# Performance work log

Hardware: AMD Instinct MI355X
Metric: run time of the kernel (lower is better)

The kernel has to match this reference:

```python
import jax, jax.numpy as jnp
import numpy as np

KER = 8  # patch size used by unfold/fold
EPS = 1e-5


def _gelu(x):
    return jax.nn.gelu(x, approximate=False)  # torch nn.GELU default (exact erf)


def _conv(x, w, b):
    # x: [B,C,H,W], w: [O,I,kh,kw]
    y = jax.lax.conv_general_dilated(x, w, (1, 1), 'SAME',
                                     dimension_numbers=('NCHW', 'OIHW', 'NCHW'))
    return y + b[None, :, None, None]


def _unfold_t(x):
    # F.unfold(k=8, s=8).transpose(1,2): [B,C,H,W] -> [B, L, C*k*k]
    B, C, H, W = x.shape
    Hp, Wp = H // KER, W // KER
    x = x.reshape(B, C, Hp, KER, Wp, KER)
    x = x.transpose(0, 2, 4, 1, 3, 5)  # [B,Hp,Wp,C,k,k]
    return x.reshape(B, Hp * Wp, C * KER * KER)


def _fold(y, H, W):
    # inverse of unfold (non-overlapping): [B,L,C*k*k] -> [B,C,H,W]
    B, L, D = y.shape
    Hp, Wp = H // KER, W // KER
    C = D // (KER * KER)
    y = y.reshape(B, Hp, Wp, C, KER, KER).transpose(0, 3, 1, 4, 2, 5)
    return y.reshape(B, C, H, W)


def _bn1d(x, gamma, beta):
    # BatchNorm1d (training-mode batch stats) on [B, C, L]: stats over (B, L)
    m = x.mean(axis=(0, 2), keepdims=True)
    v = x.var(axis=(0, 2), keepdims=True)  # biased variance, matches torch fwd
    return (x - m) * jax.lax.rsqrt(v + EPS) * gamma[None, :, None] + beta[None, :, None]


def setup_inputs() -> dict:
    key = jax.random.key(0)
    ks = jax.random.split(key, 12)
    B, C, H, W = 4, 64, 256, 256
    dq = KER * KER * C  # 4096

    def n(k, shape, scale=0.02):
        return jax.random.normal(k, shape, jnp.float32) * scale

    return {
        'feat': jax.random.normal(ks[0], (B, C, H, W), jnp.float32),
        'w_enc': n(ks[1], (C, C, 3, 3)), 'b_enc': jnp.zeros((C,), jnp.float32),
        'w_kc': n(ks[2], (C, C, 3, 3)), 'b_kc': jnp.zeros((C,), jnp.float32),
        'w_vc': n(ks[3], (C, C, 3, 3)), 'b_vc': jnp.zeros((C,), jnp.float32),
        'wq': n(ks[4], (1024, dq)), 'bq': jnp.zeros((1024,), jnp.float32),
        'wk': n(ks[5], (1024, dq)), 'bk': jnp.zeros((1024,), jnp.float32),
        'gq': jnp.ones((1024,), jnp.float32), 'betaq': jnp.zeros((1024,), jnp.float32),
        'gk': jnp.ones((1024,), jnp.float32), 'betak': jnp.zeros((1024,), jnp.float32),
        'w_f1': n(ks[6], (4 * C, C, 1, 1)), 'b_f1': jnp.zeros((4 * C,), jnp.float32),
        'w_f2': n(ks[7], (C, 4 * C, 1, 1)), 'b_f2': jnp.zeros((C,), jnp.float32),
    }


def reference(feat, w_enc, b_enc, w_kc, b_kc, w_vc, b_vc, wq, bq, wk, bk,
              gq, betaq, gk, betak, w_f1, b_f1, w_f2, b_f2):
    H, W = feat.shape[-2:]
    refer = _gelu(_conv(feat, w_enc, b_enc))
    feat_k = _gelu(_conv(feat, w_kc, b_kc))
    feat_v = _gelu(_conv(feat, w_vc, b_vc))

    q_un = _unfold_t(refer)   # [B,L,4096]
    k_un = _unfold_t(feat_k)
    v_un = _unfold_t(feat_v)

    # Linear -> BN1d over 1024 channels (transpose dance as in the torch code)
    qp = _bn1d((q_un @ wq.T + bq).transpose(0, 2, 1), gq, betaq).transpose(0, 2, 1)  # [B,L,1024]
    kp = _bn1d((k_un @ wk.T + bk).transpose(0, 2, 1), gk, betak).transpose(0, 2, 1)  # [B,L,1024]

    scale = jnp.sqrt(jnp.asarray(qp.shape[2], qp.dtype))
    scores = jnp.einsum('bld,bmd->blm', qp, kp) / scale  # [B,L,L]
    attn = jax.nn.softmax(scores, axis=2)
    out = jnp.einsum('blm,bmd->bld', attn, v_un)  # [B,L,4096]

    out = _fold(out, H, W)  # [B,C,H,W]
    ff = _gelu(_conv(out, w_f1, b_f1))
    ff = _gelu(_conv(ff, w_f2, b_f2))
    return ff + feat
```

## Files before the change

### kernel.cpp

```cpp
#include <hip/hip_runtime.h>
#include <hip/hip_bf16.h>

typedef unsigned short u16;
typedef __attribute__((ext_vector_type(8))) short short8v;
typedef __attribute__((ext_vector_type(8))) unsigned short u16x8;
typedef __attribute__((ext_vector_type(4))) float f32x4;

#define HWPIX 65536

__device__ __forceinline__ float bfbits2f(u16 u) {
  return __uint_as_float(((unsigned)u) << 16);
}
__device__ __forceinline__ float4 ld4bf(const u16* p) {
  ushort4 u = *(const ushort4*)(const void*)p;
  return make_float4(bfbits2f(u.x), bfbits2f(u.y), bfbits2f(u.z), bfbits2f(u.w));
}
__device__ __forceinline__ u16 f2bf(float f) {
  union { __hip_bfloat16 h; u16 u; } c;
  c.h = __float2bfloat16(f);
  return c.u;
}
__device__ __forceinline__ float gelu_f(float x) {
  float z = 0.79788456f * x * (1.0f + 0.044715f * x * x);
  float e = __expf(2.0f * z);
  float th = 1.0f - 2.0f * __builtin_amdgcn_rcpf(e + 1.0f);
  return 0.5f * x * (1.0f + th);
}
__device__ __forceinline__ u16x8 bn8(u16x8 v, const float* __restrict__ sc,
                                     const float* __restrict__ sh, int kk) {
  float4 s0 = *(const float4*)&sc[kk], s1 = *(const float4*)&sc[kk + 4];
  float4 t0 = *(const float4*)&sh[kk], t1 = *(const float4*)&sh[kk + 4];
  u16x8 r;
  r[0] = f2bf(bfbits2f(v[0]) * s0.x + t0.x); r[1] = f2bf(bfbits2f(v[1]) * s0.y + t0.y);
  r[2] = f2bf(bfbits2f(v[2]) * s0.z + t0.z); r[3] = f2bf(bfbits2f(v[3]) * s0.w + t0.w);
  r[4] = f2bf(bfbits2f(v[4]) * s1.x + t1.x); r[5] = f2bf(bfbits2f(v[5]) * s1.y + t1.y);
  r[6] = f2bf(bfbits2f(v[6]) * s1.z + t1.z); r[7] = f2bf(bfbits2f(v[7]) * s1.w + t1.w);
  return r;
}

__launch_bounds__(256)
__global__ void nhwc_k(const float* __restrict__ x, u16* __restrict__ y) {
  __shared__ float tile[64][65];
  const int t = threadIdx.x;
  const int xs = blockIdx.x << 6, yy = blockIdx.y, b = blockIdx.z;
#pragma unroll
  for (int it = 0; it < 4; ++it) {
    const int idx = t + it * 256;
    const int c = idx >> 4, seg = (idx & 15) << 2;
    float4 v = *(const float4*)&x[(((size_t)(b * 64 + c)) << 16) + yy * 256 + xs + seg];
    tile[c][seg] = v.x; tile[c][seg + 1] = v.y; tile[c][seg + 2] = v.z; tile[c][seg + 3] = v.w;
  }
  __syncthreads();
#pragma unroll
  for (int it = 0; it < 4; ++it) {
    const int idx = t + it * 256;
    const int cs = (idx & 15) << 2, px = idx >> 4;
    ushort4 r;
    r.x = f2bf(tile[cs + 0][px]); r.y = f2bf(tile[cs + 1][px]);
    r.z = f2bf(tile[cs + 2][px]); r.w = f2bf(tile[cs + 3][px]);
    *(ushort4*)&y[(((size_t)((b * 256 + yy) * 256 + xs + px)) << 6) + cs] = r;
  }
}

__launch_bounds__(256)
__global__ void wcvt2_k(const float* __restrict__ s0, u16* __restrict__ d0,
                        const float* __restrict__ s1, u16* __restrict__ d1) {
  const float* src = blockIdx.y ? s1 : s0;
  u16* dst = blockIdx.y ? d1 : d0;
  const int i = (blockIdx.x * 256 + threadIdx.x) << 2;
  float4 v = *(const float4*)&src[i];
  ushort4 r;
  r.x = f2bf(v.x); r.y = f2bf(v.y); r.z = f2bf(v.z); r.w = f2bf(v.w);
  *(ushort4*)&dst[i] = r;
}

__launch_bounds__(256)
__global__ void wprep_k(const float* __restrict__ w0, const float* __restrict__ w1,
                        const float* __restrict__ w2, const float* __restrict__ b0,
                        const float* __restrict__ b1, const float* __restrict__ b2,
                        const float* __restrict__ wf1, const float* __restrict__ wf2,
                        u16* __restrict__ wT, float* __restrict__ bias192,
                        u16* __restrict__ wf1b, u16* __restrict__ wf2b) {
  const int t = threadIdx.x;
  const int bx = blockIdx.x;
  if (bx >= 497) {
    const int e = (bx - 497) * 256 + t;
    wf2b[e] = f2bf(wf2[e]);
    return;
  }
  if (bx >= 433) {
    const int e = (bx - 433) * 256 + t;
    wf1b[e] = f2bf(wf1[e]);
    return;
  }
  if (bx == 432) {
    if (t < 192) {
      const float* bp = (t < 64) ? b0 : (t < 128) ? b1 : b2;
      bias192[t] = bp[t & 63];
    }
    return;
  }
  const int e = bx * 256 + t;
  const int pos = e / 12288, rem = e % 12288;
  const int n = rem >> 6, ic = rem & 63;
  const int conv = n >> 6, oc = n & 63;
  const float* wp = (conv == 0) ? w0 : (conv == 1) ? w1 : w2;
  wT[e] = f2bf(wp[(oc * 64 + ic) * 9 + pos]);
}

__launch_bounds__(256)
__global__ void convmfma_k(const u16* __restrict__ featb, const u16* __restrict__ wT,
                           const float* __restrict__ bias192, u16* __restrict__ qun,
                           u16* __restrict__ kun, u16* __restrict__ vT) {
  __shared__ u16 As[128 * 40];
  __shared__ u16 Bs[192 * 40];
  const int tid = threadIdx.x;
  const int lin = blockIdx.x;
  const int virt = (lin & 7) * 256 + (lin >> 3);
  const int b = virt >> 9, yy = (virt >> 1) & 255, x0 = (virt & 1) << 7;
  const int lane = tid & 63, w = tid >> 6;
  const int wm = w >> 1, wn = w & 1;

  const int arow = tid >> 1, acs = (tid & 1) << 4;
  const int brow0 = tid >> 2, bseg0 = (tid & 3) << 3;

  f32x4 acc[4][6] = {};
  const int kc = (lane >> 4) << 3;
  const int afr = wm * 64 + (lane & 15);
  const int bfr0 = wn * 96 + (lane & 15);

  for (int s = 0; s < 18; ++s) {
    const int pos = s >> 1, half = (s & 1) << 5;
    const int dy = pos / 3, dx = pos % 3;
    {
      const int yp = yy + dy - 1;
      const int xp = x0 + arow + dx - 1;
      u16x8 pA0{}, pA1{};
      if ((unsigned)yp < 256u && (unsigned)xp < 256u) {
        const u16* src = featb + (((size_t)((b * 256 + yp) * 256 + xp)) << 6) + half + acs;
        pA0 = *(const u16x8*)src;
        pA1 = *(const u16x8*)(src + 8);
      }
      *(u16x8*)&As[arow * 40 + acs] = pA0;
      *(u16x8*)&As[arow * 40 + acs + 8] = pA1;
    }
    {
      const u16* wb = wT + (size_t)pos * 12288 + half;
      *(u16x8*)&Bs[(brow0 + 0) * 40 + bseg0] = *(const u16x8*)&wb[(brow0 + 0) * 64 + bseg0];
      *(u16x8*)&Bs[(brow0 + 64) * 40 + bseg0] = *(const u16x8*)&wb[(brow0 + 64) * 64 + bseg0];
      *(u16x8*)&Bs[(brow0 + 128) * 40 + bseg0] = *(const u16x8*)&wb[(brow0 + 128) * 64 + bseg0];
    }
    __syncthreads();
    short8v a[4], bf[6];
#pragma unroll
    for (int f = 0; f < 4; ++f) a[f] = *(const short8v*)&As[(afr + f * 16) * 40 + kc];
#pragma unroll
    for (int f = 0; f < 6; ++f) bf[f] = *(const short8v*)&Bs[(bfr0 + f * 16) * 40 + kc];
#pragma unroll
    for (int i = 0; i < 4; ++i)
#pragma unroll
      for (int j = 0; j < 6; ++j)
        acc[i][j] = __builtin_amdgcn_mfma_f32_16x16x32_bf16(a[i], bf[j], acc[i][j], 0, 0, 0);
    __syncthreads();
  }

  const int py = yy >> 3, ky = yy & 7;
  const int rp0 = wm * 64 + ((lane >> 4) << 2);
#pragma unroll
  for (int j = 0; j < 6; ++j) {
    const int colb = wn * 96 + j * 16;
    const int conv = colb >> 6;
    const int oc = (colb & 63) + (lane & 15);
    const float bj = bias192[colb + (lane & 15)];
#pragma unroll
    for (int i = 0; i < 4; ++i) {
      const int rp = rp0 + i * 16;
      const int xg = x0 + rp;
      const int px = xg >> 3, kx0 = xg & 7;
      float v0 = gelu_f(acc[i][j][0] + bj);
      float v1 = gelu_f(acc[i][j][1] + bj);
      float v2 = gelu_f(acc[i][j][2] + bj);
      float v3 = gelu_f(acc[i][j][3] + bj);
      const int d0 = (oc << 6) + (ky << 3) + kx0;
      if (conv < 2) {
        u16* dst = conv ? kun : qun;
        const size_t addr = (((size_t)((b << 10) + py * 32 + px)) << 12) + d0;
        ushort4 r4;
        r4.x = f2bf(v0); r4.y = f2bf(v1); r4.z = f2bf(v2); r4.w = f2bf(v3);
        *(ushort4*)&dst[addr] = r4;
      } else {
        const int m = py * 32 + px;
        const size_t base = (((size_t)(b * 4096 + d0)) << 10) + m;
        vT[base] = f2bf(v0);
        vT[base + 1024] = f2bf(v1);
        vT[base + 2048] = f2bf(v2);
        vT[base + 3072] = f2bf(v3);
      }
    }
  }
}

__launch_bounds__(256)
__global__ void bnpart_k(const u16* __restrict__ q, const u16* __restrict__ k,
                         float2* __restrict__ part) {
  const u16* x = blockIdx.y ? k : q;
  const int b = blockIdx.x, t = threadIdx.x;
  const int c = t << 2;
  float s0 = 0.f, s1 = 0.f, s2 = 0.f, s3 = 0.f;
  float q0 = 0.f, q1 = 0.f, q2 = 0.f, q3 = 0.f;
  const u16* base = x + ((size_t)b << 15) + c;
#pragma unroll 4
  for (int r = 0; r < 32; ++r) {
    float4 v = ld4bf(base + (r << 10));
    s0 += v.x; q0 += v.x * v.x;
    s1 += v.y; q1 += v.y * v.y;
    s2 += v.z; q2 += v.z * v.z;
    s3 += v.w; q3 += v.w * v.w;
  }
  float2* dst = part + (((size_t)(blockIdx.y * 128 + b)) << 10) + c;
  dst[0] = make_float2(s0, q0);
  dst[1] = make_float2(s1, q1);
  dst[2] = make_float2(s2, q2);
  dst[3] = make_float2(s3, q3);
}
__launch_bounds__(256)
__global__ void bnfin_k(const float2* __restrict__ part, const float* __restrict__ gq,
                        const float* __restrict__ betaq, const float* __restrict__ gk,
                        const float* __restrict__ betak, float* __restrict__ scq,
                        float* __restrict__ shq, float* __restrict__ sck,
                        float* __restrict__ shk) {
  const int n = blockIdx.x * 256 + threadIdx.x;
  const int y = blockIdx.y;
  const float2* p = part + (((size_t)(y * 128)) << 10) + n;
  float S = 0.f, S2 = 0.f;
  for (int i = 0; i < 128; ++i) {
    float2 v = p[(size_t)i << 10];
    S += v.x; S2 += v.y;
  }
  const float mean = S * (1.0f / 4096.0f);
  const float var = S2 * (1.0f / 4096.0f) - mean * mean;
  const float rstd = rsqrtf(var + 1e-5f);
  const float g = (y ? gk : gq)[n];
  const float be = (y ? betak : betaq)[n];
  const float sc = g * rstd;
  (y ? sck : scq)[n] = sc;
  (y ? shk : shq)[n] = be - mean * sc;
}

__launch_bounds__(256)
__global__ void softmax_k(u16* __restrict__ s) {
  u16* p = s + (size_t)blockIdx.x * 1024;
  const int tid = threadIdx.x;
  float4 v = ld4bf(p + (tid << 2));
  float mx = fmaxf(fmaxf(v.x, v.y), fmaxf(v.z, v.w));
#pragma unroll
  for (int off = 32; off > 0; off >>= 1) mx = fmaxf(mx, __shfl_xor(mx, off));
  __shared__ float red[8];
  if ((tid & 63) == 0) red[tid >> 6] = mx;
  __syncthreads();
  mx = fmaxf(fmaxf(red[0], red[1]), fmaxf(red[2], red[3]));
  float e0 = __expf(v.x - mx), e1 = __expf(v.y - mx), e2 = __expf(v.z - mx), e3 = __expf(v.w - mx);
  float sm = e0 + e1 + e2 + e3;
#pragma unroll
  for (int off = 32; off > 0; off >>= 1) sm += __shfl_xor(sm, off);
  if ((tid & 63) == 0) red[4 + (tid >> 6)] = sm;
  __syncthreads();
  sm = red[4] + red[5] + red[6] + red[7];
  float inv = 1.0f / sm;
  ushort4 r;
  r.x = f2bf(e0 * inv); r.y = f2bf(e1 * inv); r.z = f2bf(e2 * inv); r.w = f2bf(e3 * inv);
  *(ushort4*)&p[tid << 2] = r;
}

template <int MODE>
__launch_bounds__(512)
__global__ void mgemm8_k(const u16* __restrict__ Ap0, const u16* __restrict__ Bp0,
                         const float* __restrict__ sA, const float* __restrict__ hA,
                         const float* __restrict__ sB, const float* __restrict__ hB,
                         const float* __restrict__ bias0, u16* __restrict__ Cp0, int K,
                         const u16* __restrict__ Ap2, const u16* __restrict__ Bp2,
                         const float* __restrict__ bias2, u16* __restrict__ Cp2) {
  constexpr int SD = (MODE == 0) ? 4096 : 1024;
  __shared__ u16 As[2][128 * 72];
  __shared__ u16 Bs[2][128 * 72];
  const int tid = threadIdx.x;

  int bx, by, z;
  if constexpr (MODE == 2) {
    int lin = blockIdx.x + 32 * blockIdx.y + 256 * blockIdx.z;
    int sw = (lin & 7) * 128 + (lin >> 3);
    bx = sw & 31; by = (sw >> 5) & 7; z = sw >> 8;
  } else {
    bx = blockIdx.x; by = blockIdx.y; z = blockIdx.z;
  }
  const u16* Ap = Ap0;
  const u16* Bp = Bp0;
  const float* bias = bias0;
  u16* Cp = Cp0;
  if constexpr (MODE == 0) {
    if (z) { Ap = Ap2; Bp = Bp2; bias = bias2; Cp = Cp2; }
  }
  const int m0 = by * 128, n0 = bx * 128;
  const int lane = tid & 63, w = tid >> 6;
  const int wm = w >> 2, wn = w & 3;

  const int srow = tid >> 3;
  const int scol = (tid & 7) << 3;
  const size_t zoffA = (MODE == 0) ? 0 : ((size_t)z << 10);
  const size_t zoffB = (MODE == 0) ? 0 : (MODE == 1) ? ((size_t)z << 10) : ((size_t)z << 12);
  const u16* A0 = Ap + (zoffA + m0 + srow) * (size_t)SD + scol;
  const u16* A1 = A0 + (size_t)64 * SD;
  const u16* B0 = Bp + (zoffB + n0 + srow) * (size_t)SD + scol;
  const u16* B1 = B0 + (size_t)64 * SD;
  const int l0 = srow * 72 + scol;
  const int l1 = (srow + 64) * 72 + scol;

  const int NT = K >> 6;
  u16x8 pA0 = *(const u16x8*)A0;
  u16x8 pA1 = *(const u16x8*)A1;
  u16x8 pB0 = *(const u16x8*)B0;
  u16x8 pB1 = *(const u16x8*)B1;
  if constexpr (MODE == 1) {
    pA0 = bn8(pA0, sA, hA, scol); pA1 = bn8(pA1, sA, hA, scol);
    pB0 = bn8(pB0, sB, hB, scol); pB1 = bn8(pB1, sB, hB, scol);
  }
  *(u16x8*)&As[0][l0] = pA0; *(u16x8*)&As[0][l1] = pA1;
  *(u16x8*)&Bs[0][l0] = pB0; *(u16x8*)&Bs[0][l1] = pB1;
  __syncthreads();

  f32x4 acc[4][2] = {};
  int cur = 0;
  for (int t = 0; t < NT; ++t) {
    const int kn = (t + 1) << 6;
    if (t + 1 < NT) {
      pA0 = *(const u16x8*)(A0 + kn);
      pA1 = *(const u16x8*)(A1 + kn);
      pB0 = *(const u16x8*)(B0 + kn);
      pB1 = *(const u16x8*)(B1 + kn);
    }
    const u16* Asb = As[cur];
    const u16* Bsb = Bs[cur];
#pragma unroll
    for (int ks = 0; ks < 2; ++ks) {
      const int kc = ks * 32 + ((lane >> 4) << 3);
      short8v a[4], bfr[2];
#pragma unroll
      for (int f = 0; f < 4; ++f)
        a[f] = *(const short8v*)&Asb[(wm * 64 + (lane & 15) + f * 16) * 72 + kc];
#pragma unroll
      for (int f = 0; f < 2; ++f)
        bfr[f] = *(const short8v*)&Bsb[(wn * 32 + (lane & 15) + f * 16) * 72 + kc];
#pragma unroll
      for (int i = 0; i < 4; ++i)
#pragma unroll
        for (int j = 0; j < 2; ++j)
          acc[i][j] = __builtin_amdgcn_mfma_f32_16x16x32_bf16(a[i], bfr[j], acc[i][j], 0, 0, 0);
    }
    if (t + 1 < NT) {
      if constexpr (MODE == 1) {
        pA0 = bn8(pA0, sA, hA, kn + scol); pA1 = bn8(pA1, sA, hA, kn + scol);
        pB0 = bn8(pB0, sB, hB, kn + scol); pB1 = bn8(pB1, sB, hB, kn + scol);
      }
      *(u16x8*)&As[cur ^ 1][l0] = pA0; *(u16x8*)&As[cur ^ 1][l1] = pA1;
      *(u16x8*)&Bs[cur ^ 1][l0] = pB0; *(u16x8*)&Bs[cur ^ 1][l1] = pB1;
    }
    __syncthreads();
    cur ^= 1;
  }

  const int rowbase = m0 + wm * 64 + ((lane >> 4) << 2);
  const int colbase = n0 + wn * 32 + (lane & 15);
  if constexpr (MODE == 2) {
    const size_t coff = (size_t)(8 + 8 * z) * 524288;
    u16* C = Cp + coff;
#pragma unroll
    for (int j = 0; j < 2; ++j) {
      const int d = colbase + j * 16;
      const int c = d >> 6, ky = (d >> 3) & 7, kx = d & 7;
#pragma unroll
      for (int i = 0; i < 4; ++i)
#pragma unroll
        for (int r = 0; r < 4; ++r) {
          const int l = rowbase + i * 16 + r;
          const int p = (((l >> 5) << 3) + ky) * 256 + ((l & 31) << 3) + kx;
          C[((size_t)p << 6) + c] = f2bf(acc[i][j][r]);
        }
    }
  } else {
#pragma unroll
    for (int j = 0; j < 2; ++j) {
      const int col = colbase + j * 16;
      float bj = 0.f;
      if constexpr (MODE == 0) bj = bias[col];
#pragma unroll
      for (int i = 0; i < 4; ++i)
#pragma unroll
        for (int r = 0; r < 4; ++r) {
          const size_t row = (MODE == 1 ? ((size_t)z << 10) : 0) + rowbase + i * 16 + r;
          float v = (MODE == 0) ? (acc[i][j][r] + bj) : (acc[i][j][r] * 0.03125f);
          Cp[row * 1024 + col] = f2bf(v);
        }
    }
  }
}

__launch_bounds__(512)
__global__ void ffn_k(const u16* __restrict__ fold, const u16* __restrict__ w1b,
                      const u16* __restrict__ w2b, const float* __restrict__ b1,
                      const float* __restrict__ b2, const float* __restrict__ feat,
                      float* __restrict__ out) {
  extern __shared__ u16 sh[];
  u16* Ash = sh;
  u16* W1s = sh + 9216;
  u16* mids = sh;
  const int t = threadIdx.x;
  const int px0 = blockIdx.x << 7;
  const int z = blockIdx.y;
  const u16* fz = fold + ((size_t)z << 22);

  {
    const int row = t >> 2, cs = (t & 3) << 4;
    const u16* src = fz + (((size_t)(px0 + row)) << 6) + cs;
    *(u16x8*)&Ash[row * 72 + cs] = *(const u16x8*)src;
    *(u16x8*)&Ash[row * 72 + cs + 8] = *(const u16x8*)(src + 8);
  }
  {
    const int row = t >> 1, cs = (t & 1) << 5;
    const u16* src = w1b + (((size_t)row) << 6) + cs;
    *(u16x8*)&W1s[row * 72 + cs] = *(const u16x8*)src;
    *(u16x8*)&W1s[row * 72 + cs + 8] = *(const u16x8*)(src + 8);
    *(u16x8*)&W1s[row * 72 + cs + 16] = *(const u16x8*)(src + 16);
    *(u16x8*)&W1s[row * 72 + cs + 24] = *(const u16x8*)(src + 24);
  }
  __syncthreads();

  const int lane = t & 63, w = t >> 6;
  const int kc = (lane >> 4) << 3;
  const int mrow = w * 16 + (lane & 15);
  f32x4 acc1[16] = {};
  short8v a0 = *(const short8v*)&Ash[mrow * 72 + kc];
  short8v a1 = *(const short8v*)&Ash[mrow * 72 + 32 + kc];
#pragma unroll
  for (int n = 0; n < 16; ++n) {
    const int br = n * 16 + (lane & 15);
    short8v b0 = *(const short8v*)&W1s[br * 72 + kc];
    short8v bv = *(const short8v*)&W1s[br * 72 + 32 + kc];
    acc1[n] = __builtin_amdgcn_mfma_f32_16x16x32_bf16(a0, b0, acc1[n], 0, 0, 0);
    acc1[n] = __builtin_amdgcn_mfma_f32_16x16x32_bf16(a1, bv, acc1[n], 0, 0, 0);
  }
  __syncthreads();

  const int mrow0 = w * 16 + ((lane >> 4) << 2);
#pragma unroll
  for (int n = 0; n < 16; ++n) {
    const int col = n * 16 + (lane & 15);
    const float bj = b1[col];
#pragma unroll
    for (int r = 0; r < 4; ++r)
      mids[(mrow0 + r) * 264 + col] = f2bf(gelu_f(acc1[n][r] + bj));
  }
  __syncthreads();

  f32x4 acc2[4] = {};
#pragma unroll
  for (int ks = 0; ks < 8; ++ks) {
    short8v a2 = *(const short8v*)&mids[(w * 16 + (lane & 15)) * 264 + ks * 32 + kc];
#pragma unroll
    for (int n = 0; n < 4; ++n) {
      short8v bv = *(const short8v*)(const void*)&w2b[(size_t)(n * 16 + (lane & 15)) * 256 + ks * 32 + kc];
      acc2[n] = __builtin_amdgcn_mfma_f32_16x16x32_bf16(a2, bv, acc2[n], 0, 0, 0);
    }
  }
#pragma unroll
  for (int n = 0; n < 4; ++n) {
    const int oc = n * 16 + (lane & 15);
    const float bn = b2[oc];
    const int px = px0 + mrow0;
    const size_t base = (((size_t)(z * 64 + oc)) << 16) + px;
    float4 f = *(const float4*)&feat[base];
    float4 rv;
    rv.x = gelu_f(acc2[n][0] + bn) + f.x;
    rv.y = gelu_f(acc2[n][1] + bn) + f.y;
    rv.z = gelu_f(acc2[n][2] + bn) + f.z;
    rv.w = gelu_f(acc2[n][3] + bn) + f.w;
    *(float4*)&out[base] = rv;
  }
}

extern "C" void kernel_launch(void* const* d_in, const int* in_sizes, int n_in,
                              void* d_out, int out_size, void* d_ws, size_t ws_size,
                              hipStream_t stream) {
  const float* feat  = (const float*)d_in[0];
  const float* w_enc = (const float*)d_in[1];
  const float* b_enc = (const float*)d_in[2];
  const float* w_kc  = (const float*)d_in[3];
  const float* b_kc  = (const float*)d_in[4];
  const float* w_vc  = (const float*)d_in[5];
  const float* b_vc  = (const float*)d_in[6];
  const float* wq    = (const float*)d_in[7];
  const float* bq    = (const float*)d_in[8];
  const float* wk    = (const float*)d_in[9];
  const float* bk    = (const float*)d_in[10];
  const float* gq    = (const float*)d_in[11];
  const float* betaq = (const float*)d_in[12];
  const float* gk    = (const float*)d_in[13];
  const float* betak = (const float*)d_in[14];
  const float* w_f1  = (const float*)d_in[15];
  const float* b_f1  = (const float*)d_in[16];
  const float* w_f2  = (const float*)d_in[17];
  const float* b_f2  = (const float*)d_in[18];

  char* ws = (char*)d_ws;
  const size_t MB = (size_t)1 << 20;
  u16*   qun    = (u16*)(ws);
  u16*   kun    = (u16*)(ws + 32 * MB);
  u16*   qlin   = (u16*)(ws + 64 * MB);
  u16*   klin   = (u16*)(ws + 40 * MB);
  u16*   wqb    = (u16*)(ws + 72 * MB);
  u16*   wT     = (u16*)(ws + 80 * MB);
  float* bias192= (float*)(ws + 80 * MB + 224 * 1024);
  float* scaleq = (float*)(ws + 80 * MB + 232 * 1024);
  float* shiftq = scaleq + 1024;
  float* scalek = shiftq + 1024;
  float* shiftk = scalek + 1024;
  u16*   wf1b   = (u16*)(ws + 80 * MB + 512 * 1024);
  u16*   wf2b   = (u16*)(ws + 80 * MB + 576 * 1024);
  float2* bnpart = (float2*)(ws + 81 * MB);
  u16*   scores = (u16*)(ws);
  u16*   featb  = (u16*)d_out;
  u16*   vT     = (u16*)((char*)d_out + 32 * MB);
  u16*   wkb    = (u16*)d_out;

  const dim3 blk(256);
  const dim3 blk8(512);
  nhwc_k<<<dim3(4, 256, 4), blk, 0, stream>>>(feat, featb);
  wprep_k<<<561, blk, 0, stream>>>(w_enc, w_kc, w_vc, b_enc, b_kc, b_vc,
                                   w_f1, w_f2, wT, bias192, wf1b, wf2b);
  convmfma_k<<<2048, blk, 0, stream>>>(featb, wT, bias192, qun, kun, vT);
  wcvt2_k<<<dim3(4096, 2), blk, 0, stream>>>(wq, wqb, wk, wkb);
  mgemm8_k<0><<<dim3(8, 32, 2), blk8, 0, stream>>>(qun, wqb, nullptr, nullptr, nullptr, nullptr,
                                                   bq, qlin, 4096, kun, wkb, bk, klin);
  bnpart_k<<<dim3(128, 2), blk, 0, stream>>>(qlin, klin, bnpart);
  bnfin_k<<<dim3(4, 2), blk, 0, stream>>>(bnpart, gq, betaq, gk, betak, scaleq, shiftq, scalek, shiftk);
  mgemm8_k<1><<<dim3(8, 8, 4), blk8, 0, stream>>>(qlin, klin, scaleq, shiftq, scalek, shiftk,
                                                  nullptr, scores, 1024, nullptr, nullptr, nullptr, nullptr);
  softmax_k<<<4096, blk, 0, stream>>>(scores);
  mgemm8_k<2><<<dim3(32, 8, 4), blk8, 0, stream>>>(scores, vT, nullptr, nullptr, nullptr, nullptr,
                                                   nullptr, (u16*)ws, 1024, nullptr, nullptr, nullptr, nullptr);
  ffn_k<<<dim3(512, 4), blk8, 67584, stream>>>((u16*)(ws + 8 * MB), wf1b, wf2b, b_f1, b_f2, feat, (float*)d_out);
  (void)in_sizes; (void)n_in; (void)out_size; (void)ws_size;
}
```

Before: 491.5 us.

## Use direct global-to-LDS loads with XOR-swizzled tiles in projection and PV GEMMs

The GEMM kernel is split in two. The BN-fused QK^T GEMM keeps the register-staged path, now in its own kernel. The projection and attention-times-V GEMMs now move data with global_load_lds straight into LDS, which skips the register round trip and the ds_write instructions. To avoid bank conflicts without padding, the LDS tiles use an XOR swizzle on the 8-element column groups, and the synchronisation point moves to the top of each k-iteration. The risk is that correctness now depends on global_load_lds completion at the barrier and on the swizzled LDS layout matching the wave-contiguous write order.

```diff
diff --git a/kernel.cpp b/kernel.cpp
--- a/kernel.cpp
+++ b/kernel.cpp
@@ -7,6 +7,8 @@
 typedef __attribute__((ext_vector_type(4))) float f32x4;
 
 #define HWPIX 65536
+#define AS1(p) ((const __attribute__((address_space(1))) void*)(p))
+#define AS3(p) ((__attribute__((address_space(3))) void*)(p))
 
 __device__ __forceinline__ float bfbits2f(u16 u) {
   return __uint_as_float(((unsigned)u) << 16);
@@ -274,15 +276,13 @@
 
 template <int MODE>
 __launch_bounds__(512)
-__global__ void mgemm8_k(const u16* __restrict__ Ap0, const u16* __restrict__ Bp0,
-                         const float* __restrict__ sA, const float* __restrict__ hA,
-                         const float* __restrict__ sB, const float* __restrict__ hB,
+__global__ void mgemmL_k(const u16* __restrict__ Ap0, const u16* __restrict__ Bp0,
                          const float* __restrict__ bias0, u16* __restrict__ Cp0, int K,
                          const u16* __restrict__ Ap2, const u16* __restrict__ Bp2,
                          const float* __restrict__ bias2, u16* __restrict__ Cp2) {
   constexpr int SD = (MODE == 0) ? 4096 : 1024;
-  __shared__ u16 As[2][128 * 72];
-  __shared__ u16 Bs[2][128 * 72];
+  __shared__ u16 As[2][128 * 64];
+  __shared__ u16 Bs[2][128 * 64];
   const int tid = threadIdx.x;
 
   int bx, by, z;
@@ -305,25 +305,121 @@
   const int wm = w >> 2, wn = w & 3;
 
   const int srow = tid >> 3;
+  const int scol = (((tid & 7) ^ (srow & 7)) << 3);
+  const size_t zoffA = (MODE == 0) ? 0 : ((size_t)z << 10);
+  const size_t zoffB = (MODE == 0) ? 0 : ((size_t)z << 12);
+  const u16* gA0 = Ap + (zoffA + m0 + srow) * (size_t)SD + scol;
+  const u16* gA1 = gA0 + (size_t)64 * SD;
+  const u16* gB0 = Bp + (zoffB + n0 + srow) * (size_t)SD + scol;
+  const u16* gB1 = gB0 + (size_t)64 * SD;
+  const int lw0 = (w * 8) * 64;
+  const int lw1 = (64 + w * 8) * 64;
+
+  const int NT = K >> 6;
+  __builtin_amdgcn_global_load_lds(AS1(gA0), AS3(&As[0][lw0]), 16, 0, 0);
+  __builtin_amdgcn_global_load_lds(AS1(gA1), AS3(&As[0][lw1]), 16, 0, 0);
+  __builtin_amdgcn_global_load_lds(AS1(gB0), AS3(&Bs[0][lw0]), 16, 0, 0);
+  __builtin_amdgcn_global_load_lds(AS1(gB1), AS3(&Bs[0][lw1]), 16, 0, 0);
+
+  f32x4 acc[4][2] = {};
+  const int fr = lane & 15;
+  const int kg = (lane >> 4) << 3;
+  int cur = 0;
+  for (int t = 0; t < NT; ++t) {
+    __syncthreads();
+    if (t + 1 < NT) {
+      const int kn = (t + 1) << 6;
+      __builtin_amdgcn_global_load_lds(AS1(gA0 + kn), AS3(&As[cur ^ 1][lw0]), 16, 0, 0);
+      __builtin_amdgcn_global_load_lds(AS1(gA1 + kn), AS3(&As[cur ^ 1][lw1]), 16, 0, 0);
+      __builtin_amdgcn_global_load_lds(AS1(gB0 + kn), AS3(&Bs[cur ^ 1][lw0]), 16, 0, 0);
+      __builtin_amdgcn_global_load_lds(AS1(gB1 + kn), AS3(&Bs[cur ^ 1][lw1]), 16, 0, 0);
+    }
+    const u16* Asb = As[cur];
+    const u16* Bsb = Bs[cur];
+#pragma unroll
+    for (int ks = 0; ks < 2; ++ks) {
+      const int ce = ks * 32 + kg;
+      short8v a[4], bfr[2];
+#pragma unroll
+      for (int f = 0; f < 4; ++f) {
+        const int row = wm * 64 + fr + f * 16;
+        a[f] = *(const short8v*)&Asb[row * 64 + (ce ^ ((row & 7) << 3))];
+      }
+#pragma unroll
+      for (int f = 0; f < 2; ++f) {
+        const int row = wn * 32 + fr + f * 16;
+        bfr[f] = *(const short8v*)&Bsb[row * 64 + (ce ^ ((row & 7) << 3))];
+      }
+#pragma unroll
+      for (int i = 0; i < 4; ++i)
+#pragma unroll
+        for (int j = 0; j < 2; ++j)
+          acc[i][j] = __builtin_amdgcn_mfma_f32_16x16x32_bf16(a[i], bfr[j], acc[i][j], 0, 0, 0);
+    }
+    cur ^= 1;
+  }
+
+  const int rowbase = m0 + wm * 64 + ((lane >> 4) << 2);
+  const int colbase = n0 + wn * 32 + (lane & 15);
+  if constexpr (MODE == 2) {
+    const size_t coff = (size_t)(8 + 8 * z) * 524288;
+    u16* C = Cp + coff;
+#pragma unroll
+    for (int j = 0; j < 2; ++j) {
+      const int d = colbase + j * 16;
+      const int c = d >> 6, ky = (d >> 3) & 7, kx = d & 7;
+#pragma unroll
+      for (int i = 0; i < 4; ++i)
+#pragma unroll
+        for (int r = 0; r < 4; ++r) {
+          const int l = rowbase + i * 16 + r;
+          const int p = (((l >> 5) << 3) + ky) * 256 + ((l & 31) << 3) + kx;
+          C[((size_t)p << 6) + c] = f2bf(acc[i][j][r]);
+        }
+    }
+  } else {
+#pragma unroll
+    for (int j = 0; j < 2; ++j) {
+      const int col = colbase + j * 16;
+      const float bj = bias[col];
+#pragma unroll
+      for (int i = 0; i < 4; ++i)
+#pragma unroll
+        for (int r = 0; r < 4; ++r)
+          Cp[(size_t)(rowbase + i * 16 + r) * 1024 + col] = f2bf(acc[i][j][r] + bj);
+    }
+  }
+}
+
+__launch_bounds__(512)
+__global__ void mgemm1_k(const u16* __restrict__ Ap, const u16* __restrict__ Bp,
+                         const float* __restrict__ sA, const float* __restrict__ hA,
+                         const float* __restrict__ sB, const float* __restrict__ hB,
+                         u16* __restrict__ Cp, int K) {
+  constexpr int SD = 1024;
+  __shared__ u16 As[2][128 * 72];
+  __shared__ u16 Bs[2][128 * 72];
+  const int tid = threadIdx.x;
+  const int bx = blockIdx.x, by = blockIdx.y, z = blockIdx.z;
+  const int m0 = by * 128, n0 = bx * 128;
+  const int lane = tid & 63, w = tid >> 6;
+  const int wm = w >> 2, wn = w & 3;
+
+  const int srow = tid >> 3;
   const int scol = (tid & 7) << 3;
-  const size_t zoffA = (MODE == 0) ? 0 : ((size_t)z << 10);
-  const size_t zoffB = (MODE == 0) ? 0 : (MODE == 1) ? ((size_t)z << 10) : ((size_t)z << 12);
-  const u16* A0 = Ap + (zoffA + m0 + srow) * (size_t)SD + scol;
+  const size_t zoff = (size_t)z << 10;
+  const u16* A0 = Ap + (zoff + m0 + srow) * (size_t)SD + scol;
   const u16* A1 = A0 + (size_t)64 * SD;
-  const u16* B0 = Bp + (zoffB + n0 + srow) * (size_t)SD + scol;
+  const u16* B0 = Bp + (zoff + n0 + srow) * (size_t)SD + scol;
   const u16* B1 = B0 + (size_t)64 * SD;
   const int l0 = srow * 72 + scol;
   const int l1 = (srow + 64) * 72 + scol;
 
   const int NT = K >> 6;
-  u16x8 pA0 = *(const u16x8*)A0;
-  u16x8 pA1 = *(const u16x8*)A1;
-  u16x8 pB0 = *(const u16x8*)B0;
-  u16x8 pB1 = *(const u16x8*)B1;
-  if constexpr (MODE == 1) {
-    pA0 = bn8(pA0, sA, hA, scol); pA1 = bn8(pA1, sA, hA, scol);
-    pB0 = bn8(pB0, sB, hB, scol); pB1 = bn8(pB1, sB, hB, scol);
-  }
+  u16x8 pA0 = bn8(*(const u16x8*)A0, sA, hA, scol);
+  u16x8 pA1 = bn8(*(const u16x8*)A1, sA, hA, scol);
+  u16x8 pB0 = bn8(*(const u16x8*)B0, sB, hB, scol);
+  u16x8 pB1 = bn8(*(const u16x8*)B1, sB, hB, scol);
   *(u16x8*)&As[0][l0] = pA0; *(u16x8*)&As[0][l1] = pA1;
   *(u16x8*)&Bs[0][l0] = pB0; *(u16x8*)&Bs[0][l1] = pB1;
   __syncthreads();
@@ -357,10 +453,8 @@
           acc[i][j] = __builtin_amdgcn_mfma_f32_16x16x32_bf16(a[i], bfr[j], acc[i][j], 0, 0, 0);
     }
     if (t + 1 < NT) {
-      if constexpr (MODE == 1) {
-        pA0 = bn8(pA0, sA, hA, kn + scol); pA1 = bn8(pA1, sA, hA, kn + scol);
-        pB0 = bn8(pB0, sB, hB, kn + scol); pB1 = bn8(pB1, sB, hB, kn + scol);
-      }
+      pA0 = bn8(pA0, sA, hA, kn + scol); pA1 = bn8(pA1, sA, hA, kn + scol);
+      pB0 = bn8(pB0, sB, hB, kn + scol); pB1 = bn8(pB1, sB, hB, kn + scol);
       *(u16x8*)&As[cur ^ 1][l0] = pA0; *(u16x8*)&As[cur ^ 1][l1] = pA1;
       *(u16x8*)&Bs[cur ^ 1][l0] = pB0; *(u16x8*)&Bs[cur ^ 1][l1] = pB1;
     }
@@ -370,37 +464,16 @@
 
   const int rowbase = m0 + wm * 64 + ((lane >> 4) << 2);
   const int colbase = n0 + wn * 32 + (lane & 15);
-  if constexpr (MODE == 2) {
-    const size_t coff = (size_t)(8 + 8 * z) * 524288;
-    u16* C = Cp + coff;
-#pragma unroll
-    for (int j = 0; j < 2; ++j) {
-      const int d = colbase + j * 16;
-      const int c = d >> 6, ky = (d >> 3) & 7, kx = d & 7;
-#pragma unroll
-      for (int i = 0; i < 4; ++i)
-#pragma unroll
-        for (int r = 0; r < 4; ++r) {
-          const int l = rowbase + i * 16 + r;
-          const int p = (((l >> 5) << 3) + ky) * 256 + ((l & 31) << 3) + kx;
-          C[((size_t)p << 6) + c] = f2bf(acc[i][j][r]);
-        }
-    }
-  } else {
-#pragma unroll
-    for (int j = 0; j < 2; ++j) {
-      const int col = colbase + j * 16;
-      float bj = 0.f;
-      if constexpr (MODE == 0) bj = bias[col];
-#pragma unroll
-      for (int i = 0; i < 4; ++i)
-#pragma unroll
-        for (int r = 0; r < 4; ++r) {
-          const size_t row = (MODE == 1 ? ((size_t)z << 10) : 0) + rowbase + i * 16 + r;
-          float v = (MODE == 0) ? (acc[i][j][r] + bj) : (acc[i][j][r] * 0.03125f);
-          Cp[row * 1024 + col] = f2bf(v);
-        }
-    }
+#pragma unroll
+  for (int j = 0; j < 2; ++j) {
+    const int col = colbase + j * 16;
+#pragma unroll
+    for (int i = 0; i < 4; ++i)
+#pragma unroll
+      for (int r = 0; r < 4; ++r) {
+        const size_t row = ((size_t)z << 10) + rowbase + i * 16 + r;
+        Cp[row * 1024 + col] = f2bf(acc[i][j][r] * 0.03125f);
+      }
   }
 }
 
@@ -538,15 +611,15 @@
                                    w_f1, w_f2, wT, bias192, wf1b, wf2b);
   convmfma_k<<<2048, blk, 0, stream>>>(featb, wT, bias192, qun, kun, vT);
   wcvt2_k<<<dim3(4096, 2), blk, 0, stream>>>(wq, wqb, wk, wkb);
-  mgemm8_k<0><<<dim3(8, 32, 2), blk8, 0, stream>>>(qun, wqb, nullptr, nullptr, nullptr, nullptr,
-                                                   bq, qlin, 4096, kun, wkb, bk, klin);
+  mgemmL_k<0><<<dim3(8, 32, 2), blk8, 0, stream>>>(qun, wqb, bq, qlin, 4096,
+                                                   kun, wkb, bk, klin);
   bnpart_k<<<dim3(128, 2), blk, 0, stream>>>(qlin, klin, bnpart);
   bnfin_k<<<dim3(4, 2), blk, 0, stream>>>(bnpart, gq, betaq, gk, betak, scaleq, shiftq, scalek, shiftk);
-  mgemm8_k<1><<<dim3(8, 8, 4), blk8, 0, stream>>>(qlin, klin, scaleq, shiftq, scalek, shiftk,
-                                                  nullptr, scores, 1024, nullptr, nullptr, nullptr, nullptr);
+  mgemm1_k<<<dim3(8, 8, 4), blk8, 0, stream>>>(qlin, klin, scaleq, shiftq, scalek, shiftk,
+                                               scores, 1024);
   softmax_k<<<4096, blk, 0, stream>>>(scores);
-  mgemm8_k<2><<<dim3(32, 8, 4), blk8, 0, stream>>>(scores, vT, nullptr, nullptr, nullptr, nullptr,
-                                                   nullptr, (u16*)ws, 1024, nullptr, nullptr, nullptr, nullptr);
+  mgemmL_k<2><<<dim3(32, 8, 4), blk8, 0, stream>>>(scores, vT, nullptr, (u16*)ws, 1024,
+                                                   nullptr, nullptr, nullptr, nullptr);
   ffn_k<<<dim3(512, 4), blk8, 67584, stream>>>((u16*)(ws + 8 * MB), wf1b, wf2b, b_f1, b_f2, feat, (float*)d_out);
   (void)in_sizes; (void)n_in; (void)out_size; (void)ws_size;
 }
```

Result: faster. 474.8 us (-3.4%).
